# Performance work log

Measured on AMD Instinct MI355X. Metric: run time of the kernel, lower is better.

## Reference

```python
import jax, jax.numpy as jnp
import numpy as np

NMAX = 20  # matches init nmax=20 -> (NMAX+1)^2 = 441 (n,m) pairs, 882 output channels
INV_SQRT_4PI = 1.0 / np.sqrt(4.0 * np.pi)


def _normalized_assoc_legendre(x, s, nmax):
    """Fully-normalized associated Legendre Pbar_n^m(x) = sqrt((2n+1)/(4pi)*(n-m)!/(n+m)!) * P_n^m(x)
    (Condon-Shortley phase included, as in sympy's assoc_legendre). Returns dict (m,n)->array."""
    P = {(0, 0): jnp.full_like(x, INV_SQRT_4PI)}
    # diagonal: Pbar_m^m = -sqrt((2m+1)/(2m)) * s * Pbar_{m-1}^{m-1}  (minus sign = CS phase)
    for m in range(1, nmax + 1):
        P[(m, m)] = (-np.sqrt((2 * m + 1) / (2.0 * m))) * s * P[(m - 1, m - 1)]
    for m in range(0, nmax + 1):
        if m + 1 <= nmax:
            P[(m, m + 1)] = np.sqrt(2 * m + 3.0) * x * P[(m, m)]
        for n in range(m + 2, nmax + 1):
            a = np.sqrt((4.0 * n * n - 1.0) / (n * n - m * m))
            b = np.sqrt((2.0 * n + 1.0) * (n - 1 - m) * (n - 1 + m) / ((2.0 * n - 3.0) * (n * n - m * m)))
            P[(m, n)] = a * x * P[(m, n - 1)] - b * P[(m, n - 2)]
    return P


def _spherical_harmonics(theta, phi, nmax):
    # sympy Ynm(n, m, _phi, _theta): polar angle = phi input, azimuth = theta input.
    x = jnp.cos(phi)                                   # cos(polar)
    s = jnp.sqrt(jnp.clip(1.0 - x * x, 0.0, None))     # (1 - cos^2)^{1/2}, matches sympy expansion
    P = _normalized_assoc_legendre(x, s, nmax)
    cos_m = [jnp.cos(m * theta) for m in range(nmax + 1)]
    sin_m = [jnp.sin(m * theta) for m in range(nmax + 1)]
    channels = []
    for n in range(nmax + 1):
        for m in range(-n, n + 1):
            am = abs(m)
            re = P[(am, n)] * cos_m[am]
            im = P[(am, n)] * sin_m[am]
            if m < 0:  # Y_n^{-m} = (-1)^m conj(Y_n^m)
                sgn = 1.0 if am % 2 == 0 else -1.0
                re = sgn * re
                im = -sgn * im
            channels.append(re)
            channels.append(im)
    return jnp.stack(channels, axis=-1)  # [B, N, 2*(nmax+1)^2]


def setup_inputs() -> dict:
    key = jax.random.key(0)
    k1, k2 = jax.random.split(key)
    B, N = 16, 4096
    theta = jax.random.uniform(k1, (B, N), dtype=jnp.float32)
    phi = jax.random.uniform(k2, (B, N), dtype=jnp.float32)
    return {"theta": theta, "phi": phi}


def reference(theta, phi):
    return _spherical_harmonics(theta, phi, NMAX)
```

## Files before the change

### kernel.cpp

```cpp
#include <hip/hip_runtime.h>

#define NM    20
#define NP1   21
#define PTS   4
#define BLK   64
#define ROWF  882
#define BLKF  (PTS * ROWF)
#define BLKF4 (BLKF / 4)

typedef float f32x4 __attribute__((ext_vector_type(4)));
typedef float f32x2 __attribute__((ext_vector_type(2)));

struct Tbl {
    float dprod[NP1];
    float e[NP1];
    float a[NP1][NP1];
    float b[NP1][NP1];
};

constexpr double csqrt_d(double x) {
    double r = x * 0.5 + 0.5;
    for (int i = 0; i < 48; ++i) r = 0.5 * (r + x / r);
    return r;
}

constexpr Tbl make_tbl() {
    Tbl t{};
    const double inv4pi = 0.28209479177387814;
    double dp = inv4pi;
    t.dprod[0] = (float)dp;
    for (int m = 1; m <= NM; ++m) {
        dp *= -csqrt_d((2.0 * m + 1.0) / (2.0 * m));
        t.dprod[m] = (float)dp;
    }
    for (int m = 0; m <= NM; ++m) t.e[m] = (float)csqrt_d(2.0 * m + 3.0);
    for (int m = 0; m <= NM; ++m)
        for (int n = m + 2; n <= NM; ++n) {
            double nn = (double)n * n, mm = (double)m * m;
            t.a[m][n] = (float)csqrt_d((4.0 * nn - 1.0) / (nn - mm));
            t.b[m][n] = (float)csqrt_d((2.0 * n + 1.0) * (n - 1.0 - m) * (n - 1.0 + m) /
                                       ((2.0 * n - 3.0) * (nn - mm)));
        }
    return t;
}

__constant__ Tbl TBL = make_tbl();

__global__ __launch_bounds__(BLK) void sph_kernel(const float* __restrict__ theta,
                                                  const float* __restrict__ phi,
                                                  float* __restrict__ out, int npts) {
    __shared__ __align__(16) float sh[PTS][ROWF];
    const int tid = threadIdx.x;
    const int pt  = tid >> 4;
    const int sub = tid & 15;
    const int gpt0 = blockIdx.x * PTS;
    const int gpt  = gpt0 + pt;

    if (gpt < npts) {
        const float th = theta[gpt];
        const float ph = phi[gpt];
        const float x = cosf(ph);
        const float s = sqrtf(fmaxf(1.0f - x * x, 0.0f));
        float* row = sh[pt];

        auto do_col = [&](int m) {
            float sm_, cm_;
            sincosf((float)m * th, &sm_, &cm_);
            float pmm = TBL.dprod[m];
            for (int k = 0; k < m; ++k) pmm *= s;
            float pb = 0.0f, pa = pmm;
            int nn = m * (m + 1);
            for (int n = m; n <= NM; ++n) {
                const float re = pa * cm_, im = pa * sm_;
                *reinterpret_cast<float2*>(row + 2 * (nn + m)) = make_float2(re, im);
                if (m > 0) {
                    float2 v = (m & 1) ? make_float2(-re, im) : make_float2(re, -im);
                    *reinterpret_cast<float2*>(row + 2 * (nn - m)) = v;
                }
                if (n < NM) {
                    const float pn = (n == m) ? TBL.e[m] * x * pa
                                              : TBL.a[m][n + 1] * x * pa - TBL.b[m][n + 1] * pb;
                    pb = pa; pa = pn;
                }
                nn += 2 * (n + 1);
            }
        };
        do_col(sub);
        if (sub <= 4) do_col(20 - sub);
    }
    __syncthreads();

    const long long base = (long long)blockIdx.x * BLKF;
    if (gpt0 + PTS <= npts) {
        const f32x4* __restrict__ src = reinterpret_cast<const f32x4*>(&sh[0][0]);
        f32x4* __restrict__ dst = reinterpret_cast<f32x4*>(out + base);
        #pragma unroll
        for (int k = 0; k < BLKF4 / BLK; ++k)
            __builtin_nontemporal_store(src[tid + k * BLK], dst + tid + k * BLK);
        const int j = tid + (BLKF4 / BLK) * BLK;
        if (j < BLKF4) __builtin_nontemporal_store(src[j], dst + j);
    } else {
        const int vpts = npts - gpt0;
        const f32x2* __restrict__ src = reinterpret_cast<const f32x2*>(&sh[0][0]);
        f32x2* __restrict__ dst = reinterpret_cast<f32x2*>(out + base);
        for (int j = tid; j < vpts * (ROWF / 2); j += BLK)
            __builtin_nontemporal_store(src[j], dst + j);
    }
}

extern "C" void kernel_launch(void* const* d_in, const int* in_sizes, int n_in,
                              void* d_out, int out_size, void* d_ws, size_t ws_size,
                              hipStream_t stream) {
    const float* theta = (const float*)d_in[0];
    const float* phi   = (const float*)d_in[1];
    float* out = (float*)d_out;
    const int npts = in_sizes[0];
    const int blocks = (npts + PTS - 1) / PTS;
    sph_kernel<<<blocks, BLK, 0, stream>>>(theta, phi, out, npts);
}
```

Before: 66.02 us.

## Stage compact Legendre and trig tables in LDS, expand to channels during store

Instead of writing all 882 output floats per point into shared memory, each point now stores only the 231 Legendre values plus cos/sin(m·theta) in LDS. During the store phase a constant channel map reconstructs each (re, im) pair with sign flips. Blocks now hold two waves of four points each, and launch bounds request higher occupancy. This cuts LDS footprint and LDS write traffic, at the cost of gathered LDS reads and an extra multiply at store time. Global stores become 8-byte per lane, replacing the earlier 16-byte ones.

```diff
diff --git a/kernel.cpp b/kernel.cpp
--- a/kernel.cpp
+++ b/kernel.cpp
@@ -2,13 +2,15 @@
 
 #define NM    20
 #define NP1   21
-#define PTS   4
-#define BLK   64
+#define PPW   4
+#define WVS   2
+#define BLK   (WVS * 64)
+#define PPB   (PPW * WVS)
+#define TRI   231
+#define PTF   273
 #define ROWF  882
-#define BLKF  (PTS * ROWF)
-#define BLKF4 (BLKF / 4)
+#define NPAIR 441
 
-typedef float f32x4 __attribute__((ext_vector_type(4)));
 typedef float f32x2 __attribute__((ext_vector_type(2)));
 
 struct Tbl {
@@ -46,43 +48,58 @@
 
 __constant__ Tbl TBL = make_tbl();
 
-__global__ __launch_bounds__(BLK) void sph_kernel(const float* __restrict__ theta,
-                                                  const float* __restrict__ phi,
-                                                  float* __restrict__ out, int npts) {
-    __shared__ __align__(16) float sh[PTS][ROWF];
-    const int tid = threadIdx.x;
-    const int pt  = tid >> 4;
-    const int sub = tid & 15;
-    const int gpt0 = blockIdx.x * PTS;
-    const int gpt  = gpt0 + pt;
+struct CMap { unsigned short m[448]; };
+constexpr CMap make_cmap() {
+    CMap c{};
+    int ch = 0;
+    for (int n = 0; n <= NM; ++n)
+        for (int mm = -n; mm <= n; ++mm) {
+            int am = mm < 0 ? -mm : mm;
+            unsigned pidx = (unsigned)(n * (n + 1) / 2 + am);
+            unsigned negRe = (mm < 0 && (am & 1)) ? 1u : 0u;
+            unsigned negIm = (mm < 0 && !(am & 1)) ? 1u : 0u;
+            c.m[ch++] = (unsigned short)(pidx | (am << 8) | (negRe << 13) | (negIm << 14));
+        }
+    return c;
+}
+__constant__ CMap CMAP = make_cmap();
+
+__global__ __launch_bounds__(BLK, 8) void sph_kernel(const float* __restrict__ theta,
+                                                     const float* __restrict__ phi,
+                                                     float* __restrict__ out, int npts) {
+    __shared__ float sh[PPB][PTF];
+    const int tid  = threadIdx.x;
+    const int wv   = tid >> 6;
+    const int lane = tid & 63;
+    const int pt   = lane >> 4;
+    const int sub  = lane & 15;
+    const int wbase = blockIdx.x * PPB + wv * PPW;
+    const int gpt   = wbase + pt;
 
     if (gpt < npts) {
         const float th = theta[gpt];
         const float ph = phi[gpt];
         const float x = cosf(ph);
         const float s = sqrtf(fmaxf(1.0f - x * x, 0.0f));
-        float* row = sh[pt];
+        float* shp = sh[wv * PPW + pt];
 
         auto do_col = [&](int m) {
-            float sm_, cm_;
-            sincosf((float)m * th, &sm_, &cm_);
+            float sn_, cs_;
+            sincosf((float)m * th, &sn_, &cs_);
+            shp[TRI + m]        = cs_;
+            shp[TRI + NP1 + m]  = sn_;
             float pmm = TBL.dprod[m];
             for (int k = 0; k < m; ++k) pmm *= s;
             float pb = 0.0f, pa = pmm;
-            int nn = m * (m + 1);
+            int tri = m * (m + 1) / 2 + m;
             for (int n = m; n <= NM; ++n) {
-                const float re = pa * cm_, im = pa * sm_;
-                *reinterpret_cast<float2*>(row + 2 * (nn + m)) = make_float2(re, im);
-                if (m > 0) {
-                    float2 v = (m & 1) ? make_float2(-re, im) : make_float2(re, -im);
-                    *reinterpret_cast<float2*>(row + 2 * (nn - m)) = v;
-                }
+                shp[tri] = pa;
                 if (n < NM) {
                     const float pn = (n == m) ? TBL.e[m] * x * pa
                                               : TBL.a[m][n + 1] * x * pa - TBL.b[m][n + 1] * pb;
                     pb = pa; pa = pn;
                 }
-                nn += 2 * (n + 1);
+                tri += n + 1;
             }
         };
         do_col(sub);
@@ -90,21 +107,42 @@
     }
     __syncthreads();
 
-    const long long base = (long long)blockIdx.x * BLKF;
-    if (gpt0 + PTS <= npts) {
-        const f32x4* __restrict__ src = reinterpret_cast<const f32x4*>(&sh[0][0]);
-        f32x4* __restrict__ dst = reinterpret_cast<f32x4*>(out + base);
+    unsigned em[7];
+    #pragma unroll
+    for (int i = 0; i < 7; ++i) em[i] = CMAP.m[i * 64 + lane];
+
+    #pragma unroll 1
+    for (int p = 0; p < PPW; ++p) {
+        const int g = wbase + p;
+        if (g >= npts) break;
+        const float* Pt = sh[wv * PPW + p];
+        f32x2* dst = reinterpret_cast<f32x2*>(out + (long long)g * ROWF);
+
         #pragma unroll
-        for (int k = 0; k < BLKF4 / BLK; ++k)
-            __builtin_nontemporal_store(src[tid + k * BLK], dst + tid + k * BLK);
-        const int j = tid + (BLKF4 / BLK) * BLK;
-        if (j < BLKF4) __builtin_nontemporal_store(src[j], dst + j);
-    } else {
-        const int vpts = npts - gpt0;
-        const f32x2* __restrict__ src = reinterpret_cast<const f32x2*>(&sh[0][0]);
-        f32x2* __restrict__ dst = reinterpret_cast<f32x2*>(out + base);
-        for (int j = tid; j < vpts * (ROWF / 2); j += BLK)
-            __builtin_nontemporal_store(src[j], dst + j);
+        for (int i = 0; i < 6; ++i) {
+            const unsigned e = em[i];
+            const float P  = Pt[e & 255u];
+            const int am   = (e >> 8) & 31u;
+            const float cs = Pt[TRI + am];
+            const float sn = Pt[TRI + NP1 + am];
+            float re = P * cs, im = P * sn;
+            if (e & (1u << 13)) re = -re;
+            if (e & (1u << 14)) im = -im;
+            f32x2 v = {re, im};
+            __builtin_nontemporal_store(v, dst + i * 64 + lane);
+        }
+        if (lane < NPAIR - 6 * 64) {
+            const unsigned e = em[6];
+            const float P  = Pt[e & 255u];
+            const int am   = (e >> 8) & 31u;
+            const float cs = Pt[TRI + am];
+            const float sn = Pt[TRI + NP1 + am];
+            float re = P * cs, im = P * sn;
+            if (e & (1u << 13)) re = -re;
+            if (e & (1u << 14)) im = -im;
+            f32x2 v = {re, im};
+            __builtin_nontemporal_store(v, dst + 6 * 64 + lane);
+        }
     }
 }
 
@@ -115,6 +153,6 @@
     const float* phi   = (const float*)d_in[1];
     float* out = (float*)d_out;
     const int npts = in_sizes[0];
-    const int blocks = (npts + PTS - 1) / PTS;
+    const int blocks = (npts + PPB - 1) / PPB;
     sph_kernel<<<blocks, BLK, 0, stream>>>(theta, phi, out, npts);
 }
```

After: 70.17 us. 1.06x slower.
